# Kernel optimization log

Measured on AMD Instinct MI355X. Metric: run time of the kernel, lower is better.

The kernel has to match this reference:

```python
import jax, jax.numpy as jnp
import numpy as np

B, C, H, W = 8, 128, 64, 64  # dim = in_channels = 128, N = H*W = 4096
TEMP = float(C) ** 0.5


def _proj(x, w, b):
    # 1x1 conv: [B,C,H,W] x [D,C] -> [B,D,H,W]
    return jnp.einsum('bchw,dc->bdhw', x, w) + b[None, :, None, None]


def setup_inputs() -> dict:
    key = jax.random.key(0)
    ks = jax.random.split(key, 6)
    std = 0.01
    x = jax.random.normal(ks[0], (B, C, H, W), dtype=jnp.float32)
    wq = jax.random.normal(ks[1], (C, C), dtype=jnp.float32) * std
    wk = jax.random.normal(ks[2], (C, C), dtype=jnp.float32) * std
    wv = jax.random.normal(ks[3], (C, C), dtype=jnp.float32) * std
    wo = jax.random.normal(ks[4], (C, C), dtype=jnp.float32) * std
    zeros = jnp.zeros((C,), dtype=jnp.float32)
    return {"x": x, "wq": wq, "bq": zeros, "wk": wk, "bk": zeros,
            "wv": wv, "bv": zeros, "wo": wo, "bo": zeros}


def reference(x, wq, bq, wk, bk, wv, bv, wo, bo):
    n, c, h, w = x.shape
    N = h * w
    q = _proj(x, wq, bq).reshape(n, c, N)          # [B, D, N]
    k = _proj(x, wk, bk).reshape(n, c, N)          # [B, D, N]
    v = _proj(x, wv, bv).reshape(n, c, N)          # [B, D, N]
    # attn[b, i, j] = sum_d q[b,d,i] * k[b,d,j] / temp
    attn = jnp.einsum('bdi,bdj->bij', q, k) / TEMP  # [B, N, N]
    attn = jax.nn.softmax(attn, axis=-1)
    # y[b, d, i] = sum_j attn[b,i,j] * v[b,d,j]
    y = jnp.einsum('bij,bdj->bdi', attn, v).reshape(n, c, h, w)
    y = _proj(y, wo, bo)                            # conv_out
    return x + y                                    # identity residual
```

## Files before the change

kernel.cpp:

```cpp
#include <hip/hip_runtime.h>


typedef float  f32x4  __attribute__((ext_vector_type(4)));
typedef float  f32x16 __attribute__((ext_vector_type(16)));
typedef short  s16x8  __attribute__((ext_vector_type(8)));
typedef short  s16x4  __attribute__((ext_vector_type(4)));
typedef unsigned uint4v __attribute__((ext_vector_type(4)));

#define MFMA16(A, Bb, Cc) __builtin_amdgcn_mfma_f32_16x16x32_bf16(A, Bb, Cc, 0, 0, 0)
#define MFMA32(A, Bb, Cc) __builtin_amdgcn_mfma_f32_32x32x16_bf16(A, Bb, Cc, 0, 0, 0)

#define BATCH 8
#define DIM   128
#define NN    4096
#define NSPLIT 4
#define JCHUNK (NN / NSPLIT)
#define Q_SCALE 0.12751649736784776f

__device__ __forceinline__ unsigned short f2bf(float f) {
  union { float f; unsigned u; } v; v.f = f;
  unsigned r = v.u + 0x7FFFu + ((v.u >> 16) & 1u);
  return (unsigned short)(r >> 16);
}
__device__ __forceinline__ float bf2f(unsigned short h) {
  union { unsigned u; float f; } v; v.u = ((unsigned)h) << 16;
  return v.f;
}

__global__ __launch_bounds__(256) void wconv_kernel(
    const float* __restrict__ wq, const float* __restrict__ wk,
    const float* __restrict__ wv, const float* __restrict__ wo,
    unsigned short* __restrict__ dst) {
  int idx = blockIdx.x * 256 + threadIdx.x;
  int m = idx >> 14, off = idx & 16383;
  const float* src = (m == 0) ? wq : (m == 1) ? wk : (m == 2) ? wv : wo;
  dst[idx] = f2bf(src[off]);
}

__global__ __launch_bounds__(256) void qkv_kernel(
    const float* __restrict__ x,
    const float* __restrict__ bq, const float* __restrict__ bk,
    const float* __restrict__ bv,
    const unsigned short* __restrict__ wbf,
    unsigned short* __restrict__ qt,
    unsigned short* __restrict__ kt,
    unsigned short* __restrict__ vv) {
  __shared__ unsigned short xs[64 * 136];
  const int b = blockIdx.y;
  const int i0 = blockIdx.x * 64;
  const int z = blockIdx.z;
  const int tid = threadIdx.x;

  for (int idx = tid; idx < 2048; idx += 256) {
    int c = idx >> 4, i4 = idx & 15;
    float4 val = *(const float4*)(x + ((size_t)(b * DIM + c)) * NN + i0 + i4 * 4);
    xs[(i4 * 4 + 0) * 136 + c] = f2bf(val.x);
    xs[(i4 * 4 + 1) * 136 + c] = f2bf(val.y);
    xs[(i4 * 4 + 2) * 136 + c] = f2bf(val.z);
    xs[(i4 * 4 + 3) * 136 + c] = f2bf(val.w);
  }
  __syncthreads();

  const int w = tid >> 6, lane = tid & 63, quad = lane >> 4, l15 = lane & 15;
  const int iloc = w * 16 + l15;

  s16x8 bfrag[4];
#pragma unroll
  for (int ch = 0; ch < 4; ch++)
    bfrag[ch] = *(const s16x8*)(&xs[iloc * 136 + ch * 32 + quad * 8]);

  const int i = i0 + iloc;
  const unsigned short* wbase = wbf + z * 16384;
  const float* bias = (z == 0) ? bq : (z == 1) ? bk : bv;
  const float sc = (z == 0) ? Q_SCALE : 1.0f;

  for (int t = 0; t < 8; t++) {
    const int dl = t * 16;
    f32x4 acc = {0.f, 0.f, 0.f, 0.f};
#pragma unroll
    for (int ch = 0; ch < 4; ch++) {
      s16x8 af = *(const s16x8*)(wbase + (dl + l15) * DIM + ch * 32 + quad * 8);
      acc = MFMA16(af, bfrag[ch], acc);
    }
    if (z < 2) {
      unsigned short* dstb = (z == 0) ? qt : kt;
      s16x4 o;
#pragma unroll
      for (int r = 0; r < 4; r++) {
        int d = dl + quad * 4 + r;
        o[r] = (short)f2bf((acc[r] + bias[d]) * sc);
      }
      *(s16x4*)(dstb + ((size_t)b * NN + i) * DIM + dl + quad * 4) = o;
    } else {
#pragma unroll
      for (int r = 0; r < 4; r++) {
        int d = dl + quad * 4 + r;
        vv[((size_t)b * DIM + d) * NN + i] = f2bf(acc[r] + bias[d]);
      }
    }
  }
}

__global__ __launch_bounds__(256, 2) void attn_kernel(
    const unsigned short* __restrict__ qt,
    const unsigned short* __restrict__ kt,
    const unsigned short* __restrict__ vv,
    unsigned short* __restrict__ o_part,
    float* __restrict__ l_part) {
  __shared__ unsigned short sh[16384];
  const int b = blockIdx.y;
  const int i0 = blockIdx.x * 128;
  const int split = blockIdx.z;
  const int jbase = split * JCHUNK;
  const int tid = threadIdx.x;
  const int w = tid >> 6, lane = tid & 63;
  const int l31 = lane & 31, h = lane >> 5;

  const unsigned short* kb = kt + (size_t)b * NN * DIM;
  const unsigned short* vb = vv + (size_t)b * DIM * NN;

  s16x8 qfrag[8];
  {
    const unsigned short* qrow =
        qt + ((size_t)b * NN + i0 + w * 32 + l31) * DIM + h * 8;
#pragma unroll
    for (int kc = 0; kc < 8; kc++)
      qfrag[kc] = *(const s16x8*)(qrow + kc * 16);
  }

  f32x16 acc[4];
#pragma unroll
  for (int mt = 0; mt < 4; mt++)
#pragma unroll
    for (int e = 0; e < 16; e++) acc[mt][e] = 0.f;
  float l_acc = 0.f;

  const int kr = tid >> 4, kc_ = tid & 15;
  const int vr = tid >> 3, vc = tid & 7;
  const int vch0 = (vc & 1) ? (vc - 1) : vc;
  const int vch1 = (vc & 1) ? vc : (vc + 1);
  const int vpos = (vc & 1) * 4;

  s16x8 kpre[4], vpre[4];
#pragma unroll
  for (int it = 0; it < 4; it++) {
    kpre[it] = *(const s16x8*)(kb + (size_t)(jbase + it * 16 + kr) * DIM + kc_ * 8);
    vpre[it] = *(const s16x8*)(vb + (size_t)(it * 32 + vr) * NN + jbase + vc * 8);
  }

  for (int j0 = jbase; j0 < jbase + JCHUNK; j0 += 64) {
    __syncthreads();
#pragma unroll
    for (int it = 0; it < 4; it++) {
      const int r = it * 16 + kr;
      *(s16x8*)(sh + (((r << 4) + (kc_ ^ (r & 15))) << 3)) = kpre[it];
      const int r2 = it * 32 + vr;
      union { s16x8 v8; s16x4 v4[2]; } sp; sp.v8 = vpre[it];
      *(s16x4*)(sh + 8192 + (((r2 << 3) + (vch0 ^ (r2 & 7))) << 3) + vpos) = sp.v4[0];
      *(s16x4*)(sh + 8192 + (((r2 << 3) + (vch1 ^ (r2 & 7))) << 3) + vpos) = sp.v4[1];
    }
    __syncthreads();

    if (j0 + 64 < jbase + JCHUNK) {
      const int jn = j0 + 64;
#pragma unroll
      for (int it = 0; it < 4; it++) {
        kpre[it] = *(const s16x8*)(kb + (size_t)(jn + it * 16 + kr) * DIM + kc_ * 8);
        vpre[it] = *(const s16x8*)(vb + (size_t)(it * 32 + vr) * NN + jn + vc * 8);
      }
    }

#pragma unroll
    for (int jt = 0; jt < 2; jt++) {
      f32x16 S;
#pragma unroll
      for (int e = 0; e < 16; e++) S[e] = 0.f;
      const int j = jt * 32 + l31;
#pragma unroll
      for (int kc = 0; kc < 8; kc++) {
        s16x8 kf = *(const s16x8*)(sh + (((j << 4) + ((2 * kc + h) ^ (j & 15))) << 3));
        S = MFMA32(kf, qfrag[kc], S);
      }
      unsigned pk[8];
#pragma unroll
      for (int p = 0; p < 8; p++) {
        float e0 = exp2f(S[2 * p]), e1 = exp2f(S[2 * p + 1]);
        l_acc += e0 + e1;
        union { float f; unsigned u; } u0, u1; u0.f = e0; u1.f = e1;
        pk[p] = __builtin_amdgcn_perm(u1.u, u0.u, 0x07060302u);
      }
#pragma unroll
      for (int bl = 0; bl < 2; bl++) {
        union { uint4v u; s16x8 v; } pu;
        pu.u[0] = pk[4 * bl + 0]; pu.u[1] = pk[4 * bl + 1];
        pu.u[2] = pk[4 * bl + 2]; pu.u[3] = pk[4 * bl + 3];
        const s16x8 pf = pu.v;
        const int c0 = (jt * 2 + bl) * 2 + h;
#pragma unroll
        for (int mt = 0; mt < 4; mt++) {
          const int d = mt * 32 + l31;
          s16x8 vf = *(const s16x8*)(sh + 8192 + (((d << 3) + (c0 ^ (d & 7))) << 3));
          acc[mt] = MFMA32(vf, pf, acc[mt]);
        }
      }
    }
  }

  const float l_tot = l_acc + __shfl_xor(l_acc, 32, 64);

  __syncthreads();
  unsigned short* ep = sh + w * 4096;
#pragma unroll
  for (int mt = 0; mt < 4; mt++)
#pragma unroll
    for (int reg = 0; reg < 16; reg++) {
      int d = mt * 32 + (reg & 3) + 8 * (reg >> 2) + 4 * h;
      int dc = d >> 3;
      ep[(l31 << 7) + ((dc ^ (l31 & 15)) << 3) + (d & 7)] = f2bf(acc[mt][reg]);
    }
  __syncthreads();
#pragma unroll
  for (int it = 0; it < 8; it++) {
    int qr = it * 4 + (lane >> 4), cr = lane & 15;
    s16x8 v = *(const s16x8*)(ep + (qr << 7) + ((cr ^ (qr & 15)) << 3));
    *(s16x8*)(o_part + (((size_t)split * BATCH + b) * NN + i0 + w * 32 + qr) * DIM +
              cr * 8) = v;
  }
  if (lane < 32)
    l_part[((size_t)split * BATCH + b) * NN + i0 + w * 32 + lane] = l_tot;
}

__global__ __launch_bounds__(128) void outp_kernel(
    const float* __restrict__ x,
    const unsigned short* __restrict__ wobf,
    const float* __restrict__ bo,
    const unsigned short* __restrict__ o_part,
    const float* __restrict__ l_part,
    float* __restrict__ out) {
  const int b = blockIdx.y;
  const int tid = threadIdx.x;
  const int w = tid >> 6, lane = tid & 63, quad = lane >> 4, l15 = lane & 15;
  const int i = blockIdx.x * 32 + w * 16 + l15;

  float l = 0.f;
#pragma unroll
  for (int s = 0; s < NSPLIT; s++) l += l_part[((size_t)s * BATCH + b) * NN + i];
  const float inv = 1.0f / l;

  s16x8 bfrag[4];
#pragma unroll
  for (int ch = 0; ch < 4; ch++) {
    float o[8] = {0.f, 0.f, 0.f, 0.f, 0.f, 0.f, 0.f, 0.f};
#pragma unroll
    for (int s = 0; s < NSPLIT; s++) {
      s16x8 ov = *(const s16x8*)(o_part + (((size_t)s * BATCH + b) * NN + i) * DIM +
                                 ch * 32 + quad * 8);
#pragma unroll
      for (int jj = 0; jj < 8; jj++) o[jj] += bf2f((unsigned short)ov[jj]);
    }
    s16x8 f;
#pragma unroll
    for (int jj = 0; jj < 8; jj++) f[jj] = (short)f2bf(o[jj] * inv);
    bfrag[ch] = f;
  }

  for (int t = 0; t < 8; t++) {
    f32x4 acc = {0.f, 0.f, 0.f, 0.f};
#pragma unroll
    for (int ch = 0; ch < 4; ch++) {
      s16x8 af = *(const s16x8*)(wobf + (t * 16 + l15) * DIM + ch * 32 + quad * 8);
      acc = MFMA16(af, bfrag[ch], acc);
    }
#pragma unroll
    for (int r = 0; r < 4; r++) {
      int d = t * 16 + quad * 4 + r;
      size_t idx = ((size_t)b * DIM + d) * NN + i;
      out[idx] = x[idx] + acc[r] + bo[d];
    }
  }
}

extern "C" void kernel_launch(void* const* d_in, const int* in_sizes, int n_in,
                              void* d_out, int out_size, void* d_ws, size_t ws_size,
                              hipStream_t stream) {
  const float* x  = (const float*)d_in[0];
  const float* wq = (const float*)d_in[1];
  const float* bq = (const float*)d_in[2];
  const float* wk = (const float*)d_in[3];
  const float* bk = (const float*)d_in[4];
  const float* wv = (const float*)d_in[5];
  const float* bv = (const float*)d_in[6];
  const float* wo = (const float*)d_in[7];
  const float* bo = (const float*)d_in[8];
  float* out = (float*)d_out;

  unsigned short* ws  = (unsigned short*)d_ws;
  unsigned short* wbf = ws;
  unsigned short* qt  = ws + 65536;
  unsigned short* kt  = qt + (size_t)BATCH * NN * DIM;
  unsigned short* vv  = kt + (size_t)BATCH * NN * DIM;
  unsigned short* o_part = vv + (size_t)BATCH * NN * DIM;
  float* l_part = (float*)(o_part + (size_t)NSPLIT * BATCH * NN * DIM);

  hipLaunchKernelGGL(wconv_kernel, dim3(256), dim3(256), 0, stream, wq, wk, wv, wo, wbf);
  hipLaunchKernelGGL(qkv_kernel, dim3(64, 8, 3), dim3(256), 0, stream,
                     x, bq, bk, bv, wbf, qt, kt, vv);
  hipLaunchKernelGGL(attn_kernel, dim3(32, 8, NSPLIT), dim3(256), 0, stream,
                     qt, kt, vv, o_part, l_part);
  hipLaunchKernelGGL(outp_kernel, dim3(128, 8), dim3(128), 0, stream,
                     x, wbf + 49152, bo, o_part, l_part, out);
}
```

Measured before the change: 214.8 us.

## Process two query tiles per wave in attention to reuse K/V fragments

```diff
diff --git a/kernel.cpp b/kernel.cpp
--- a/kernel.cpp
+++ b/kernel.cpp
@@ -45,7 +45,7 @@
     unsigned short* __restrict__ qt,
     unsigned short* __restrict__ kt,
     unsigned short* __restrict__ vv) {
-  __shared__ unsigned short xs[64 * 136];
+  __shared__ float xs[DIM * 68];
   const int b = blockIdx.y;
   const int i0 = blockIdx.x * 64;
   const int z = blockIdx.z;
@@ -54,10 +54,10 @@
   for (int idx = tid; idx < 2048; idx += 256) {
     int c = idx >> 4, i4 = idx & 15;
     float4 val = *(const float4*)(x + ((size_t)(b * DIM + c)) * NN + i0 + i4 * 4);
-    xs[(i4 * 4 + 0) * 136 + c] = f2bf(val.x);
-    xs[(i4 * 4 + 1) * 136 + c] = f2bf(val.y);
-    xs[(i4 * 4 + 2) * 136 + c] = f2bf(val.z);
-    xs[(i4 * 4 + 3) * 136 + c] = f2bf(val.w);
+    xs[c * 68 + i4 * 4 + 0] = val.x;
+    xs[c * 68 + i4 * 4 + 1] = val.y;
+    xs[c * 68 + i4 * 4 + 2] = val.z;
+    xs[c * 68 + i4 * 4 + 3] = val.w;
   }
   __syncthreads();
 
@@ -66,8 +66,15 @@
 
   s16x8 bfrag[4];
 #pragma unroll
-  for (int ch = 0; ch < 4; ch++)
-    bfrag[ch] = *(const s16x8*)(&xs[iloc * 136 + ch * 32 + quad * 8]);
+  for (int ch = 0; ch < 4; ch++) {
+    s16x8 f;
+#pragma unroll
+    for (int jj = 0; jj < 8; jj++) {
+      int c = ch * 32 + quad * 8 + jj;
+      f[jj] = (short)f2bf(xs[c * 68 + iloc]);
+    }
+    bfrag[ch] = f;
+  }
 
   const int i = i0 + iloc;
   const unsigned short* wbase = wbf + z * 16384;
@@ -109,7 +116,7 @@
     float* __restrict__ l_part) {
   __shared__ unsigned short sh[16384];
   const int b = blockIdx.y;
-  const int i0 = blockIdx.x * 128;
+  const int i0 = blockIdx.x * 256;
   const int split = blockIdx.z;
   const int jbase = split * JCHUNK;
   const int tid = threadIdx.x;
@@ -119,21 +126,24 @@
   const unsigned short* kb = kt + (size_t)b * NN * DIM;
   const unsigned short* vb = vv + (size_t)b * DIM * NN;
 
-  s16x8 qfrag[8];
-  {
+  s16x8 qfrag[2][8];
+#pragma unroll
+  for (int n = 0; n < 2; n++) {
     const unsigned short* qrow =
-        qt + ((size_t)b * NN + i0 + w * 32 + l31) * DIM + h * 8;
+        qt + ((size_t)b * NN + i0 + w * 64 + n * 32 + l31) * DIM + h * 8;
 #pragma unroll
     for (int kc = 0; kc < 8; kc++)
-      qfrag[kc] = *(const s16x8*)(qrow + kc * 16);
-  }
-
-  f32x16 acc[4];
-#pragma unroll
-  for (int mt = 0; mt < 4; mt++)
-#pragma unroll
-    for (int e = 0; e < 16; e++) acc[mt][e] = 0.f;
-  float l_acc = 0.f;
+      qfrag[n][kc] = *(const s16x8*)(qrow + kc * 16);
+  }
+
+  f32x16 acc[2][4];
+#pragma unroll
+  for (int n = 0; n < 2; n++)
+#pragma unroll
+    for (int mt = 0; mt < 4; mt++)
+#pragma unroll
+      for (int e = 0; e < 16; e++) acc[n][mt][e] = 0.f;
+  float l_acc0 = 0.f, l_acc1 = 0.f;
 
   const int kr = tid >> 4, kc_ = tid & 15;
   const int vr = tid >> 3, vc = tid & 7;
@@ -141,14 +151,13 @@
   const int vch1 = (vc & 1) ? vc : (vc + 1);
   const int vpos = (vc & 1) * 4;
 
-  s16x8 kpre[4], vpre[4];
-#pragma unroll
-  for (int it = 0; it < 4; it++) {
-    kpre[it] = *(const s16x8*)(kb + (size_t)(jbase + it * 16 + kr) * DIM + kc_ * 8);
-    vpre[it] = *(const s16x8*)(vb + (size_t)(it * 32 + vr) * NN + jbase + vc * 8);
-  }
-
   for (int j0 = jbase; j0 < jbase + JCHUNK; j0 += 64) {
+    s16x8 kpre[4], vpre[4];
+#pragma unroll
+    for (int it = 0; it < 4; it++) {
+      kpre[it] = *(const s16x8*)(kb + (size_t)(j0 + it * 16 + kr) * DIM + kc_ * 8);
+      vpre[it] = *(const s16x8*)(vb + (size_t)(it * 32 + vr) * NN + j0 + vc * 8);
+    }
     __syncthreads();
 #pragma unroll
     for (int it = 0; it < 4; it++) {
@@ -161,73 +170,79 @@
     }
     __syncthreads();
 
-    if (j0 + 64 < jbase + JCHUNK) {
-      const int jn = j0 + 64;
-#pragma unroll
-      for (int it = 0; it < 4; it++) {
-        kpre[it] = *(const s16x8*)(kb + (size_t)(jn + it * 16 + kr) * DIM + kc_ * 8);
-        vpre[it] = *(const s16x8*)(vb + (size_t)(it * 32 + vr) * NN + jn + vc * 8);
-      }
-    }
-
 #pragma unroll
     for (int jt = 0; jt < 2; jt++) {
-      f32x16 S;
-#pragma unroll
-      for (int e = 0; e < 16; e++) S[e] = 0.f;
+      f32x16 S0, S1;
+#pragma unroll
+      for (int e = 0; e < 16; e++) { S0[e] = 0.f; S1[e] = 0.f; }
       const int j = jt * 32 + l31;
 #pragma unroll
       for (int kc = 0; kc < 8; kc++) {
         s16x8 kf = *(const s16x8*)(sh + (((j << 4) + ((2 * kc + h) ^ (j & 15))) << 3));
-        S = MFMA32(kf, qfrag[kc], S);
-      }
-      unsigned pk[8];
+        S0 = MFMA32(kf, qfrag[0][kc], S0);
+        S1 = MFMA32(kf, qfrag[1][kc], S1);
+      }
+      unsigned pk0[8], pk1[8];
 #pragma unroll
       for (int p = 0; p < 8; p++) {
-        float e0 = exp2f(S[2 * p]), e1 = exp2f(S[2 * p + 1]);
-        l_acc += e0 + e1;
-        union { float f; unsigned u; } u0, u1; u0.f = e0; u1.f = e1;
-        pk[p] = __builtin_amdgcn_perm(u1.u, u0.u, 0x07060302u);
+        float a0 = exp2f(S0[2 * p]), a1 = exp2f(S0[2 * p + 1]);
+        float b0 = exp2f(S1[2 * p]), b1 = exp2f(S1[2 * p + 1]);
+        l_acc0 += a0 + a1;
+        l_acc1 += b0 + b1;
+        union { float f; unsigned u; } x0, x1, y0, y1;
+        x0.f = a0; x1.f = a1; y0.f = b0; y1.f = b1;
+        pk0[p] = __builtin_amdgcn_perm(x1.u, x0.u, 0x07060302u);
+        pk1[p] = __builtin_amdgcn_perm(y1.u, y0.u, 0x07060302u);
       }
 #pragma unroll
       for (int bl = 0; bl < 2; bl++) {
-        union { uint4v u; s16x8 v; } pu;
-        pu.u[0] = pk[4 * bl + 0]; pu.u[1] = pk[4 * bl + 1];
-        pu.u[2] = pk[4 * bl + 2]; pu.u[3] = pk[4 * bl + 3];
-        const s16x8 pf = pu.v;
+        union { uint4v u; s16x8 v; } p0, p1;
+#pragma unroll
+        for (int q4 = 0; q4 < 4; q4++) {
+          p0.u[q4] = pk0[4 * bl + q4];
+          p1.u[q4] = pk1[4 * bl + q4];
+        }
+        const s16x8 pf0 = p0.v, pf1 = p1.v;
         const int c0 = (jt * 2 + bl) * 2 + h;
 #pragma unroll
         for (int mt = 0; mt < 4; mt++) {
           const int d = mt * 32 + l31;
           s16x8 vf = *(const s16x8*)(sh + 8192 + (((d << 3) + (c0 ^ (d & 7))) << 3));
-          acc[mt] = MFMA32(vf, pf, acc[mt]);
+          acc[0][mt] = MFMA32(vf, pf0, acc[0][mt]);
+          acc[1][mt] = MFMA32(vf, pf1, acc[1][mt]);
         }
       }
     }
   }
 
-  const float l_tot = l_acc + __shfl_xor(l_acc, 32, 64);
+  const float l_tot0 = l_acc0 + __shfl_xor(l_acc0, 32, 64);
+  const float l_tot1 = l_acc1 + __shfl_xor(l_acc1, 32, 64);
 
   __syncthreads();
   unsigned short* ep = sh + w * 4096;
 #pragma unroll
-  for (int mt = 0; mt < 4; mt++)
-#pragma unroll
-    for (int reg = 0; reg < 16; reg++) {
-      int d = mt * 32 + (reg & 3) + 8 * (reg >> 2) + 4 * h;
-      int dc = d >> 3;
-      ep[(l31 << 7) + ((dc ^ (l31 & 15)) << 3) + (d & 7)] = f2bf(acc[mt][reg]);
-    }
-  __syncthreads();
-#pragma unroll
-  for (int it = 0; it < 8; it++) {
-    int qr = it * 4 + (lane >> 4), cr = lane & 15;
-    s16x8 v = *(const s16x8*)(ep + (qr << 7) + ((cr ^ (qr & 15)) << 3));
-    *(s16x8*)(o_part + (((size_t)split * BATCH + b) * NN + i0 + w * 32 + qr) * DIM +
-              cr * 8) = v;
-  }
-  if (lane < 32)
-    l_part[((size_t)split * BATCH + b) * NN + i0 + w * 32 + lane] = l_tot;
+  for (int n = 0; n < 2; n++) {
+#pragma unroll
+    for (int mt = 0; mt < 4; mt++)
+#pragma unroll
+      for (int reg = 0; reg < 16; reg++) {
+        int d = mt * 32 + (reg & 3) + 8 * (reg >> 2) + 4 * h;
+        int dc = d >> 3;
+        ep[(l31 << 7) + ((dc ^ (l31 & 15)) << 3) + (d & 7)] = f2bf(acc[n][mt][reg]);
+      }
+#pragma unroll
+    for (int it = 0; it < 8; it++) {
+      int qr = it * 4 + (lane >> 4), cr = lane & 15;
+      s16x8 v = *(const s16x8*)(ep + (qr << 7) + ((cr ^ (qr & 15)) << 3));
+      *(s16x8*)(o_part +
+                (((size_t)split * BATCH + b) * NN + i0 + w * 64 + n * 32 + qr) * DIM +
+                cr * 8) = v;
+    }
+  }
+  if (lane < 32) {
+    l_part[((size_t)split * BATCH + b) * NN + i0 + w * 64 + lane] = l_tot0;
+    l_part[((size_t)split * BATCH + b) * NN + i0 + w * 64 + 32 + lane] = l_tot1;
+  }
 }
 
 __global__ __launch_bounds__(128) void outp_kernel(
@@ -305,7 +320,7 @@
   hipLaunchKernelGGL(wconv_kernel, dim3(256), dim3(256), 0, stream, wq, wk, wv, wo, wbf);
   hipLaunchKernelGGL(qkv_kernel, dim3(64, 8, 3), dim3(256), 0, stream,
                      x, bq, bk, bv, wbf, qt, kt, vv);
-  hipLaunchKernelGGL(attn_kernel, dim3(32, 8, NSPLIT), dim3(256), 0, stream,
+  hipLaunchKernelGGL(attn_kernel, dim3(16, 8, NSPLIT), dim3(256), 0, stream,
                      qt, kt, vv, o_part, l_part);
   hipLaunchKernelGGL(outp_kernel, dim3(128, 8), dim3(128), 0, stream,
                      x, wbf + 49152, bo, o_part, l_part, out);
```

Result: slower. 316.7 us (+47.4%).
